# Optimization experiments

Hardware: AMD Instinct MI355X
Metric: run time of the kernel (lower is better)

The kernel has to match this reference:

```python
import jax, jax.numpy as jnp
import numpy as np
import math

D_MODEL = 1024
H = 16
D_K = D_MODEL // H
D_FF = 4096
EPS = 1e-6


def layer_norm(x, gamma, beta):
    # torch LayerNorm-variant: unbiased std, eps added to std (not var)
    mean = jnp.mean(x, axis=-1, keepdims=True)
    std = jnp.std(x, axis=-1, keepdims=True, ddof=1)
    return gamma * (x - mean) / (std + EPS) + beta


def mha(x, mask, w_q, w_k, w_v, w_o):
    B, S, _ = x.shape
    # torch Linear (no bias): y = x @ W.T
    q = (x @ w_q.T).reshape(B, S, H, D_K).transpose(0, 2, 1, 3)
    k = (x @ w_k.T).reshape(B, S, H, D_K).transpose(0, 2, 1, 3)
    v = (x @ w_v.T).reshape(B, S, H, D_K).transpose(0, 2, 1, 3)
    scores = jnp.einsum('bhqd,bhkd->bhqk', q, k) / math.sqrt(D_K)
    scores = jnp.where(mask == 0, jnp.float32(-1e9), scores)
    attn = jax.nn.softmax(scores, axis=-1)
    out = jnp.einsum('bhqk,bhkd->bhqd', attn, v)
    out = out.transpose(0, 2, 1, 3).reshape(B, S, D_MODEL)
    return out @ w_o.T


def setup_inputs() -> dict:
    key = jax.random.key(0)
    ks = jax.random.split(key, 12)
    B, S = 4, 2048
    s = 0.02
    return {
        'x': jax.random.normal(ks[0], (B, S, D_MODEL), jnp.float32),
        'src_mask': jnp.ones((B, 1, 1, S), jnp.int32),
        'w_q': jax.random.normal(ks[1], (D_MODEL, D_MODEL), jnp.float32) * s,
        'w_k': jax.random.normal(ks[2], (D_MODEL, D_MODEL), jnp.float32) * s,
        'w_v': jax.random.normal(ks[3], (D_MODEL, D_MODEL), jnp.float32) * s,
        'w_o': jax.random.normal(ks[4], (D_MODEL, D_MODEL), jnp.float32) * s,
        'w1': jax.random.normal(ks[5], (D_FF, D_MODEL), jnp.float32) * s,
        'b1': jnp.zeros((D_FF,), jnp.float32),
        'w2': jax.random.normal(ks[6], (D_MODEL, D_FF), jnp.float32) * s,
        'b2': jnp.zeros((D_MODEL,), jnp.float32),
        'gamma1': jnp.ones((D_MODEL,), jnp.float32),
        'beta1': jnp.zeros((D_MODEL,), jnp.float32),
        'gamma2': jnp.ones((D_MODEL,), jnp.float32),
        'beta2': jnp.zeros((D_MODEL,), jnp.float32),
    }


def reference(x, src_mask, w_q, w_k, w_v, w_o, w1, b1, w2, b2,
              gamma1, beta1, gamma2, beta2):
    # AddNorm1: x + MHA(LN(x))  (pre-norm, dropout=0)
    x = x + mha(layer_norm(x, gamma1, beta1), src_mask, w_q, w_k, w_v, w_o)
    # AddNorm2: x + FFN(LN(x))
    h = layer_norm(x, gamma2, beta2)
    ffn = jax.nn.relu(h @ w1.T + b1) @ w2.T + b2
    return x + ffn
```

## Files before the change

kernel.cpp:

```cpp
#include <hip/hip_runtime.h>

#define D_MODEL 1024
#define NH 16
#define DK 64
#define DFF 4096
#define SEQ 2048
#define BATCH 4
#define NROWS (BATCH*SEQ)
#define CHUNK 2048
#define NCHUNK (NROWS/CHUNK)

typedef short bf16x8 __attribute__((ext_vector_type(8)));
typedef float f32x4 __attribute__((ext_vector_type(4)));

__device__ __forceinline__ float bf2f(unsigned short u){
  union { float f; unsigned int i; } x; x.i = ((unsigned int)u) << 16; return x.f;
}
__device__ __forceinline__ unsigned short f2bf(float f){
  union { float f; unsigned int i; } x; x.f = f;
  unsigned int r = x.i + 0x7fffu + ((x.i >> 16) & 1u);
  return (unsigned short)(r >> 16);
}
__device__ __forceinline__ float fexp2(float x){
#if __has_builtin(__builtin_amdgcn_exp2f)
  return __builtin_amdgcn_exp2f(x);
#else
  return __exp2f(x);
#endif
}

__device__ __forceinline__ void gl_lds16(const void* g, void* l) {
  __builtin_amdgcn_global_load_lds((const __attribute__((address_space(1))) void*)g,
                                   (__attribute__((address_space(3))) void*)l, 16, 0, 0);
}

__global__ __launch_bounds__(256) void cvt_f2b(const float* __restrict__ in,
                                               unsigned short* __restrict__ out, int n)
{
  int i = (blockIdx.x * 256 + threadIdx.x) * 4;
  if (i < n) {
    float4 f = *(const float4*)(in + i);
    union { int2 v; unsigned short u[4]; } o;
    o.u[0] = f2bf(f.x); o.u[1] = f2bf(f.y); o.u[2] = f2bf(f.z); o.u[3] = f2bf(f.w);
    *(int2*)(out + i) = o.v;
  }
}

__global__ __launch_bounds__(256) void ln_kernel(const float* __restrict__ in,
    const float* __restrict__ gam, const float* __restrict__ bet,
    unsigned short* __restrict__ out)
{
  const int row = blockIdx.x, t = threadIdx.x;
  const int base = t * 4;
  float4 raw = *(const float4*)(in + (size_t)row * D_MODEL + base);
  float v[4] = { raw.x, raw.y, raw.z, raw.w };
  float s  = v[0] + v[1] + v[2] + v[3];
  float s2 = v[0]*v[0] + v[1]*v[1] + v[2]*v[2] + v[3]*v[3];
  #pragma unroll
  for (int off = 32; off > 0; off >>= 1) {
    s  += __shfl_down(s,  off);
    s2 += __shfl_down(s2, off);
  }
  __shared__ float red[10];
  const int wid = t >> 6, lane = t & 63;
  if (lane == 0) { red[wid] = s; red[4 + wid] = s2; }
  __syncthreads();
  if (t == 0) {
    float ts  = red[0] + red[1] + red[2] + red[3];
    float ts2 = red[4] + red[5] + red[6] + red[7];
    float mean = ts * (1.0f / D_MODEL);
    float var  = (ts2 - (float)D_MODEL * mean * mean) * (1.0f / (D_MODEL - 1));
    var = fmaxf(var, 0.0f);
    red[8] = mean;
    red[9] = 1.0f / (sqrtf(var) + 1e-6f);
  }
  __syncthreads();
  const float mean = red[8], inv = red[9];
  float4 g4 = *(const float4*)(gam + base);
  float4 b4 = *(const float4*)(bet + base);
  union { int2 v; unsigned short u[4]; } o;
  o.u[0] = f2bf(g4.x * (v[0] - mean) * inv + b4.x);
  o.u[1] = f2bf(g4.y * (v[1] - mean) * inv + b4.y);
  o.u[2] = f2bf(g4.z * (v[2] - mean) * inv + b4.z);
  o.u[3] = f2bf(g4.w * (v[3] - mean) * inv + b4.w);
  *(int2*)(out + (size_t)row * D_MODEL + base) = o.v;
}

__global__ __launch_bounds__(256) void gemm_bt(
    const unsigned short* __restrict__ A,
    const unsigned short* __restrict__ Bw,
    int K, int N, int sA, int sB,
    const float* __restrict__ bias,
    int relu,
    const float* __restrict__ residf,
    unsigned short* __restrict__ outb,
    float* __restrict__ outf,
    float* __restrict__ atomf,
    unsigned short* __restrict__ outq,
    unsigned short* __restrict__ outk,
    unsigned short* __restrict__ outvt)
{
  __shared__ __attribute__((aligned(16))) short sAm[128 * 32];
  __shared__ __attribute__((aligned(16))) short sBm[128 * 32];
  const int t = threadIdx.x;
  const int tileN = blockIdx.x * 128;
  const int tileM = blockIdx.y * 128;
  const int kz = blockIdx.z;
  const size_t koff = (size_t)kz * K;
  const int wid = t >> 6, lane = t & 63;
  const int wM = (wid >> 1) * 64, wN = (wid & 1) * 64;
  const int quad = lane >> 4, lrow = lane & 15;

  f32x4 acc[4][4] = {};

  for (int k0 = 0; k0 < K; k0 += 32) {
    #pragma unroll
    for (int it = 0; it < 2; it++) {
      int seg = it * 256 + t;
      int row = seg >> 2, c8 = (seg & 3) * 8;
      gl_lds16(A  + (size_t)(tileM + row) * sA + koff + k0 + c8, &sAm[seg * 8]);
      gl_lds16(Bw + (size_t)(tileN + row) * sB + koff + k0 + c8, &sBm[seg * 8]);
    }
    __syncthreads();
    bf16x8 af[4], bfr[4];
    #pragma unroll
    for (int i = 0; i < 4; i++) {
      af[i]  = *(const bf16x8*)&sAm[(wM + i * 16 + lrow) * 32 + quad * 8];
      bfr[i] = *(const bf16x8*)&sBm[(wN + i * 16 + lrow) * 32 + quad * 8];
    }
    #pragma unroll
    for (int i = 0; i < 4; i++)
      #pragma unroll
      for (int j = 0; j < 4; j++)
        acc[i][j] = __builtin_amdgcn_mfma_f32_16x16x32_bf16(af[i], bfr[j], acc[i][j], 0, 0, 0);
    __syncthreads();
  }

  unsigned short* qk_out = nullptr;
  int qkv_cat = 0;
  if (outq) {
    qkv_cat = tileN >> 10;
    qk_out = (qkv_cat == 0) ? outq : outk;
  }

  #pragma unroll
  for (int i = 0; i < 4; i++) {
    #pragma unroll
    for (int j = 0; j < 4; j++) {
      const int col  = tileN + wN + j * 16 + lrow;
      const int row0 = tileM + wM + i * 16 + quad * 4;
      const float bv = (bias && kz == 0) ? bias[col] : 0.0f;
      float vals[4];
      #pragma unroll
      for (int r = 0; r < 4; r++) {
        float val = acc[i][j][r] + bv;
        if (relu) val = fmaxf(val, 0.0f);
        if (residf) val += residf[(size_t)(row0 + r) * N + col];
        vals[r] = val;
      }
      if (outq) {
        const int lcol = col & 1023;
        if (qkv_cat < 2) {
          #pragma unroll
          for (int r = 0; r < 4; r++)
            qk_out[(size_t)(row0 + r) * D_MODEL + lcol] = f2bf(vals[r]);
        } else {
          union { int2 v; unsigned short u[4]; } pk;
          #pragma unroll
          for (int r = 0; r < 4; r++) pk.u[r] = f2bf(vals[r]);
          size_t tidx = (((size_t)(row0 >> 11) * NH + (lcol >> 6)) * DK + (lcol & 63)) * SEQ + (row0 & 2047);
          *(int2*)(outvt + tidx) = pk.v;
        }
      } else if (atomf) {
        #pragma unroll
        for (int r = 0; r < 4; r++)
          atomicAdd(&atomf[(size_t)(row0 + r) * N + col], vals[r]);
      } else {
        #pragma unroll
        for (int r = 0; r < 4; r++) {
          const size_t idx = (size_t)(row0 + r) * N + col;
          if (outf) outf[idx] = vals[r];
          if (outb) outb[idx] = f2bf(vals[r]);
        }
      }
    }
  }
}

#define AQT 64
#define AKT 64
__global__ __launch_bounds__(256) void attn_mfma(
    const unsigned short* __restrict__ Qg,
    const unsigned short* __restrict__ Kg,
    const unsigned short* __restrict__ Vt,
    const int* __restrict__ mask,
    unsigned short* __restrict__ Og)
{
  __shared__ __attribute__((aligned(16))) short Ks[AKT * 64];
  __shared__ __attribute__((aligned(16))) short Vs[DK * 64];
  __shared__ __attribute__((aligned(16))) short Ps[AQT * 64];
  __shared__ __attribute__((aligned(16))) float maddf[AKT];

  const int bid = blockIdx.x;
  const int nqt = SEQ / AQT;
  const int b  = bid / (NH * nqt);
  const int h  = (bid / nqt) % NH;
  const int q0 = (bid % nqt) * AQT;
  const int t  = threadIdx.x;
  const int wv = t >> 6, lane = t & 63;
  const int quad = lane >> 4, l15 = lane & 15;
  const int sw = (l15 & 7) << 3;
  const float SCL = 0.125f * 1.44269504f;

  bf16x8 qf0, qf1;
  {
    const unsigned short* qrow = Qg + (size_t)(b * SEQ + q0 + wv * 16 + l15) * D_MODEL + h * DK;
    qf0 = *(const bf16x8*)(qrow + quad * 8);
    qf1 = *(const bf16x8*)(qrow + 32 + quad * 8);
  }
  f32x4 oacc[4] = {};
  float m_run = -1e30f, l_run = 0.0f;

  const unsigned short* Kbase = Kg + (size_t)(b * SEQ) * D_MODEL + h * DK;
  const unsigned short* Vbase = Vt + ((size_t)(b * NH + h) * DK) * SEQ;

  for (int kt = 0; kt < SEQ; kt += AKT) {
    #pragma unroll
    for (int it = 0; it < 2; it++) {
      int s = it * 256 + t;
      int row = s >> 3;
      int scol = ((s & 7) * 8) ^ ((row & 7) << 3);
      gl_lds16(Kbase + (size_t)(kt + row) * D_MODEL + scol, &Ks[s * 8]);
      gl_lds16(Vbase + (size_t)row * SEQ + kt + scol, &Vs[s * 8]);
    }
    if (t < AKT) maddf[t] = mask[b * SEQ + kt + t] ? 0.0f : -1.0e9f;
    __syncthreads();

    f32x4 sc[4];
    #pragma unroll
    for (int ct = 0; ct < 4; ct++) {
      const int krow = ct * 16 + l15;
      bf16x8 kb0 = *(const bf16x8*)&Ks[krow * 64 + ((quad * 8) ^ sw)];
      bf16x8 kb1 = *(const bf16x8*)&Ks[krow * 64 + ((32 + quad * 8) ^ sw)];
      f32x4 a = {};
      a = __builtin_amdgcn_mfma_f32_16x16x32_bf16(kb0, qf0, a, 0, 0, 0);
      a = __builtin_amdgcn_mfma_f32_16x16x32_bf16(kb1, qf1, a, 0, 0, 0);
      f32x4 md = *(const f32x4*)&maddf[ct * 16 + quad * 4];
      #pragma unroll
      for (int r = 0; r < 4; r++) a[r] = a[r] * SCL + md[r];
      sc[ct] = a;
    }

    float tmax = sc[0][0];
    #pragma unroll
    for (int ct = 0; ct < 4; ct++)
      #pragma unroll
      for (int r = 0; r < 4; r++) tmax = fmaxf(tmax, sc[ct][r]);
    tmax = fmaxf(tmax, __shfl_xor(tmax, 16));
    tmax = fmaxf(tmax, __shfl_xor(tmax, 32));

    if (!__all(tmax - m_run <= 11.5415603f)) {
      float mn = fmaxf(m_run, tmax);
      float alpha = fexp2(m_run - mn);
      m_run = mn;
      l_run *= alpha;
      float a4[4];
      #pragma unroll
      for (int r = 0; r < 4; r++) a4[r] = __shfl(alpha, quad * 4 + r);
      #pragma unroll
      for (int dt = 0; dt < 4; dt++)
        #pragma unroll
        for (int r = 0; r < 4; r++) oacc[dt][r] *= a4[r];
    }

    const int prow = wv * 16 + l15;
    float rs = 0.0f;
    #pragma unroll
    for (int ct = 0; ct < 4; ct++) {
      float p0 = fexp2(sc[ct][0] - m_run);
      float p1 = fexp2(sc[ct][1] - m_run);
      float p2 = fexp2(sc[ct][2] - m_run);
      float p3 = fexp2(sc[ct][3] - m_run);
      rs += (p0 + p1) + (p2 + p3);
      unsigned int lo, hi;
      asm("v_cvt_pk_bf16_f32 %0, %1, %2" : "=v"(lo) : "v"(p0), "v"(p1));
      asm("v_cvt_pk_bf16_f32 %0, %1, %2" : "=v"(hi) : "v"(p2), "v"(p3));
      int2 pv; pv.x = (int)lo; pv.y = (int)hi;
      *(int2*)&Ps[prow * 64 + ((ct * 16 + quad * 4) ^ sw)] = pv;
    }
    rs += __shfl_xor(rs, 16);
    rs += __shfl_xor(rs, 32);
    l_run += rs;

    bf16x8 pf0 = *(const bf16x8*)&Ps[prow * 64 + ((quad * 8) ^ sw)];
    bf16x8 pf1 = *(const bf16x8*)&Ps[prow * 64 + ((32 + quad * 8) ^ sw)];
    #pragma unroll
    for (int dt = 0; dt < 4; dt++) {
      const int vrow = dt * 16 + l15;
      bf16x8 vb0 = *(const bf16x8*)&Vs[vrow * 64 + ((quad * 8) ^ sw)];
      bf16x8 vb1 = *(const bf16x8*)&Vs[vrow * 64 + ((32 + quad * 8) ^ sw)];
      oacc[dt] = __builtin_amdgcn_mfma_f32_16x16x32_bf16(pf0, vb0, oacc[dt], 0, 0, 0);
      oacc[dt] = __builtin_amdgcn_mfma_f32_16x16x32_bf16(pf1, vb1, oacc[dt], 0, 0, 0);
    }
    __syncthreads();
  }

  float li = 1.0f / l_run;
  float linv4[4];
  #pragma unroll
  for (int r = 0; r < 4; r++) linv4[r] = __shfl(li, quad * 4 + r);
  #pragma unroll
  for (int dt = 0; dt < 4; dt++)
    #pragma unroll
    for (int r = 0; r < 4; r++)
      Og[(size_t)(b * SEQ + q0 + wv * 16 + quad * 4 + r) * D_MODEL + h * DK + dt * 16 + l15] =
        f2bf(oacc[dt][r] * linv4[r]);
}

extern "C" void kernel_launch(void* const* d_in, const int* in_sizes, int n_in,
                              void* d_out, int out_size, void* d_ws, size_t ws_size,
                              hipStream_t stream)
{
  (void)in_sizes; (void)n_in; (void)out_size; (void)ws_size;
  const float* x   = (const float*)d_in[0];
  const int*   msk = (const int*)d_in[1];
  const float* w_q = (const float*)d_in[2];
  const float* w_k = (const float*)d_in[3];
  const float* w_v = (const float*)d_in[4];
  const float* w_o = (const float*)d_in[5];
  const float* w1  = (const float*)d_in[6];
  const float* b1  = (const float*)d_in[7];
  const float* w2  = (const float*)d_in[8];
  const float* b2  = (const float*)d_in[9];
  const float* g1  = (const float*)d_in[10];
  const float* be1 = (const float*)d_in[11];
  const float* g2  = (const float*)d_in[12];
  const float* be2 = (const float*)d_in[13];
  float* outf = (float*)d_out;

  char* ws = (char*)d_ws;
  const size_t MB = 1024 * 1024;
  unsigned short* q_b  = (unsigned short*)(ws + 0);
  unsigned short* k_b  = (unsigned short*)(ws + 16 * MB);
  unsigned short* vt_b = (unsigned short*)(ws + 32 * MB);
  unsigned short* wo16 = (unsigned short*)(ws + 16 * MB);
  unsigned short* w116 = (unsigned short*)(ws + 0);
  unsigned short* w216 = (unsigned short*)(ws + 8 * MB);
  unsigned short* ln2b = vt_b;
  unsigned short* hffc = k_b;

  unsigned short* ln1b   = (unsigned short*)d_out;
  unsigned short* wqkv16 = (unsigned short*)d_out + 8 * 1024 * 1024;

  dim3 blk(256);
  const int nw = D_MODEL * D_MODEL;
  const int nf = DFF * D_MODEL;

  cvt_f2b<<<nw / 1024, blk, 0, stream>>>(w_q, wqkv16, nw);
  cvt_f2b<<<nw / 1024, blk, 0, stream>>>(w_k, wqkv16 + nw, nw);
  cvt_f2b<<<nw / 1024, blk, 0, stream>>>(w_v, wqkv16 + 2 * nw, nw);
  ln_kernel<<<NROWS, blk, 0, stream>>>(x, g1, be1, ln1b);

  dim3 gqkv(3 * D_MODEL / 128, NROWS / 128);
  gemm_bt<<<gqkv, blk, 0, stream>>>(ln1b, wqkv16, D_MODEL, 3 * D_MODEL, D_MODEL, D_MODEL,
                                    nullptr, 0, nullptr, nullptr, nullptr, nullptr,
                                    q_b, k_b, vt_b);

  attn_mfma<<<BATCH * NH * (SEQ / AQT), blk, 0, stream>>>(q_b, k_b, vt_b, msk, q_b);

  cvt_f2b<<<nw / 1024, blk, 0, stream>>>(w_o, wo16, nw);
  dim3 gN1024(D_MODEL / 128, NROWS / 128);
  gemm_bt<<<gN1024, blk, 0, stream>>>(q_b, wo16, D_MODEL, D_MODEL, D_MODEL, D_MODEL,
                                      nullptr, 0, x, nullptr, outf, nullptr,
                                      nullptr, nullptr, nullptr);

  cvt_f2b<<<nf / 1024, blk, 0, stream>>>(w1, w116, nf);
  cvt_f2b<<<nf / 1024, blk, 0, stream>>>(w2, w216, nf);
  ln_kernel<<<NROWS, blk, 0, stream>>>(outf, g2, be2, ln2b);
  for (int c = 0; c < NCHUNK; c++) {
    const size_t ro = (size_t)c * CHUNK;
    dim3 g1c(DFF / 128,     CHUNK / 128);
    dim3 g2c(D_MODEL / 128, CHUNK / 128, 4);
    gemm_bt<<<g1c, blk, 0, stream>>>(ln2b + ro * D_MODEL, w116, D_MODEL, DFF,
                                     D_MODEL, D_MODEL, b1, 1,
                                     nullptr, hffc, nullptr, nullptr,
                                     nullptr, nullptr, nullptr);
    gemm_bt<<<g2c, blk, 0, stream>>>(hffc, w216, DFF / 4, D_MODEL, DFF, DFF, b2, 0,
                                     nullptr, nullptr, nullptr, outf + ro * D_MODEL,
                                     nullptr, nullptr, nullptr);
  }
}
```

Baseline: 774.3 us.

## Double-buffer GEMM LDS, swizzle blocks across XCDs, read attention K/V directly

After: 1.044 ms. 1.35x slower.

```diff
diff --git a/kernel.cpp b/kernel.cpp
--- a/kernel.cpp
+++ b/kernel.cpp
@@ -34,6 +34,10 @@
                                    (__attribute__((address_space(3))) void*)l, 16, 0, 0);
 }
 
+__device__ __forceinline__ int xcd_swz(int hid, int total) {
+  return (hid & 7) * (total >> 3) + (hid >> 3);
+}
+
 __global__ __launch_bounds__(256) void cvt_f2b(const float* __restrict__ in,
                                                unsigned short* __restrict__ out, int n)
 {
@@ -44,6 +48,13 @@
     o.u[0] = f2bf(f.x); o.u[1] = f2bf(f.y); o.u[2] = f2bf(f.z); o.u[3] = f2bf(f.w);
     *(int2*)(out + i) = o.v;
   }
+}
+
+__global__ __launch_bounds__(256) void mask2f(const int* __restrict__ m,
+                                              float* __restrict__ o, int n)
+{
+  int i = blockIdx.x * 256 + threadIdx.x;
+  if (i < n) o[i] = m[i] ? 0.0f : -1.0e9f;
 }
 
 __global__ __launch_bounds__(256) void ln_kernel(const float* __restrict__ in,
@@ -86,7 +97,7 @@
   *(int2*)(out + (size_t)row * D_MODEL + base) = o.v;
 }
 
-__global__ __launch_bounds__(256) void gemm_bt(
+__global__ __launch_bounds__(256, 4) void gemm_bt(
     const unsigned short* __restrict__ A,
     const unsigned short* __restrict__ Bw,
     int K, int N, int sA, int sB,
@@ -100,11 +111,15 @@
     unsigned short* __restrict__ outk,
     unsigned short* __restrict__ outvt)
 {
-  __shared__ __attribute__((aligned(16))) short sAm[128 * 32];
-  __shared__ __attribute__((aligned(16))) short sBm[128 * 32];
+  __shared__ __attribute__((aligned(16))) short sA0[128 * 32];
+  __shared__ __attribute__((aligned(16))) short sA1[128 * 32];
+  __shared__ __attribute__((aligned(16))) short sB0[128 * 32];
+  __shared__ __attribute__((aligned(16))) short sB1[128 * 32];
   const int t = threadIdx.x;
-  const int tileN = blockIdx.x * 128;
-  const int tileM = blockIdx.y * 128;
+  const int lid  = xcd_swz(blockIdx.y * gridDim.x + blockIdx.x,
+                           gridDim.x * gridDim.y);
+  const int tileN = (lid % gridDim.x) * 128;
+  const int tileM = (lid / gridDim.x) * 128;
   const int kz = blockIdx.z;
   const size_t koff = (size_t)kz * K;
   const int wid = t >> 6, lane = t & 63;
@@ -113,26 +128,40 @@
 
   f32x4 acc[4][4] = {};
 
-  for (int k0 = 0; k0 < K; k0 += 32) {
-    #pragma unroll
-    for (int it = 0; it < 2; it++) {
-      int seg = it * 256 + t;
-      int row = seg >> 2, c8 = (seg & 3) * 8;
-      gl_lds16(A  + (size_t)(tileM + row) * sA + koff + k0 + c8, &sAm[seg * 8]);
-      gl_lds16(Bw + (size_t)(tileN + row) * sB + koff + k0 + c8, &sBm[seg * 8]);
-    }
-    __syncthreads();
+  const unsigned short* pa = A  + (size_t)(tileM + (t >> 2)) * sA + koff + (t & 3) * 8;
+  const unsigned short* pb = Bw + (size_t)(tileN + (t >> 2)) * sB + koff + (t & 3) * 8;
+  const size_t a64 = (size_t)64 * sA, b64 = (size_t)64 * sB;
+
+  auto stageTo = [&](short* dA, short* dB) {
+    gl_lds16(pa,       dA + t * 8);
+    gl_lds16(pa + a64, dA + (256 + t) * 8);
+    gl_lds16(pb,       dB + t * 8);
+    gl_lds16(pb + b64, dB + (256 + t) * 8);
+    pa += 32; pb += 32;
+  };
+  auto compute = [&](const short* cA, const short* cB) {
     bf16x8 af[4], bfr[4];
     #pragma unroll
     for (int i = 0; i < 4; i++) {
-      af[i]  = *(const bf16x8*)&sAm[(wM + i * 16 + lrow) * 32 + quad * 8];
-      bfr[i] = *(const bf16x8*)&sBm[(wN + i * 16 + lrow) * 32 + quad * 8];
+      af[i]  = *(const bf16x8*)&cA[(wM + i * 16 + lrow) * 32 + quad * 8];
+      bfr[i] = *(const bf16x8*)&cB[(wN + i * 16 + lrow) * 32 + quad * 8];
     }
     #pragma unroll
     for (int i = 0; i < 4; i++)
       #pragma unroll
       for (int j = 0; j < 4; j++)
         acc[i][j] = __builtin_amdgcn_mfma_f32_16x16x32_bf16(af[i], bfr[j], acc[i][j], 0, 0, 0);
+  };
+
+  const int nk = K >> 5;
+  stageTo(sA0, sB0);
+  __syncthreads();
+  for (int ik = 0; ik < nk; ik += 2) {
+    if (ik + 1 < nk) stageTo(sA1, sB1);
+    compute(sA0, sB0);
+    __syncthreads();
+    if (ik + 2 < nk) stageTo(sA0, sB0);
+    compute(sA1, sB1);
     __syncthreads();
   }
 
@@ -193,15 +222,12 @@
     const unsigned short* __restrict__ Qg,
     const unsigned short* __restrict__ Kg,
     const unsigned short* __restrict__ Vt,
-    const int* __restrict__ mask,
+    const float* __restrict__ maddg,
     unsigned short* __restrict__ Og)
 {
-  __shared__ __attribute__((aligned(16))) short Ks[AKT * 64];
-  __shared__ __attribute__((aligned(16))) short Vs[DK * 64];
-  __shared__ __attribute__((aligned(16))) short Ps[AQT * 64];
-  __shared__ __attribute__((aligned(16))) float maddf[AKT];
-
-  const int bid = blockIdx.x;
+  __shared__ __attribute__((aligned(16))) short Ps[64 * 64];
+
+  const int bid = xcd_swz(blockIdx.x, gridDim.x);
   const int nqt = SEQ / AQT;
   const int b  = bid / (NH * nqt);
   const int h  = (bid / nqt) % NH;
@@ -214,48 +240,42 @@
 
   bf16x8 qf0, qf1;
   {
-    const unsigned short* qrow = Qg + (size_t)(b * SEQ + q0 + wv * 16 + l15) * D_MODEL + h * DK;
+    const unsigned short* qrow =
+        Qg + (size_t)(b * SEQ + q0 + wv * 16 + l15) * D_MODEL + h * DK;
     qf0 = *(const bf16x8*)(qrow + quad * 8);
     qf1 = *(const bf16x8*)(qrow + 32 + quad * 8);
   }
   f32x4 oacc[4] = {};
   float m_run = -1e30f, l_run = 0.0f;
 
-  const unsigned short* Kbase = Kg + (size_t)(b * SEQ) * D_MODEL + h * DK;
-  const unsigned short* Vbase = Vt + ((size_t)(b * NH + h) * DK) * SEQ;
+  const unsigned short* kfrag =
+      Kg + (size_t)(b * SEQ + l15) * D_MODEL + h * DK + quad * 8;
+  const unsigned short* vfrag =
+      Vt + ((size_t)(b * NH + h) * DK + l15) * SEQ + quad * 8;
+  const float* mg = maddg + b * SEQ + quad * 4;
+  const int prow = wv * 16 + l15;
 
   for (int kt = 0; kt < SEQ; kt += AKT) {
-    #pragma unroll
-    for (int it = 0; it < 2; it++) {
-      int s = it * 256 + t;
-      int row = s >> 3;
-      int scol = ((s & 7) * 8) ^ ((row & 7) << 3);
-      gl_lds16(Kbase + (size_t)(kt + row) * D_MODEL + scol, &Ks[s * 8]);
-      gl_lds16(Vbase + (size_t)row * SEQ + kt + scol, &Vs[s * 8]);
-    }
-    if (t < AKT) maddf[t] = mask[b * SEQ + kt + t] ? 0.0f : -1.0e9f;
-    __syncthreads();
-
     f32x4 sc[4];
     #pragma unroll
     for (int ct = 0; ct < 4; ct++) {
-      const int krow = ct * 16 + l15;
-      bf16x8 kb0 = *(const bf16x8*)&Ks[krow * 64 + ((quad * 8) ^ sw)];
-      bf16x8 kb1 = *(const bf16x8*)&Ks[krow * 64 + ((32 + quad * 8) ^ sw)];
+      const unsigned short* kr = kfrag + (size_t)(kt + ct * 16) * D_MODEL;
+      bf16x8 kb0 = *(const bf16x8*)(kr);
+      bf16x8 kb1 = *(const bf16x8*)(kr + 32);
       f32x4 a = {};
       a = __builtin_amdgcn_mfma_f32_16x16x32_bf16(kb0, qf0, a, 0, 0, 0);
       a = __builtin_amdgcn_mfma_f32_16x16x32_bf16(kb1, qf1, a, 0, 0, 0);
-      f32x4 md = *(const f32x4*)&maddf[ct * 16 + quad * 4];
+      f32x4 md = *(const f32x4*)(mg + kt + ct * 16);
       #pragma unroll
       for (int r = 0; r < 4; r++) a[r] = a[r] * SCL + md[r];
       sc[ct] = a;
     }
 
-    float tmax = sc[0][0];
-    #pragma unroll
-    for (int ct = 0; ct < 4; ct++)
-      #pragma unroll
-      for (int r = 0; r < 4; r++) tmax = fmaxf(tmax, sc[ct][r]);
+    float tmax = fmaxf(fmaxf(sc[0][0], sc[0][1]), fmaxf(sc[0][2], sc[0][3]));
+    #pragma unroll
+    for (int ct = 1; ct < 4; ct++)
+      tmax = fmaxf(tmax, fmaxf(fmaxf(sc[ct][0], sc[ct][1]),
+                               fmaxf(sc[ct][2], sc[ct][3])));
     tmax = fmaxf(tmax, __shfl_xor(tmax, 16));
     tmax = fmaxf(tmax, __shfl_xor(tmax, 32));
 
@@ -273,7 +293,6 @@
         for (int r = 0; r < 4; r++) oacc[dt][r] *= a4[r];
     }
 
-    const int prow = wv * 16 + l15;
     float rs = 0.0f;
     #pragma unroll
     for (int ct = 0; ct < 4; ct++) {
@@ -296,13 +315,12 @@
     bf16x8 pf1 = *(const bf16x8*)&Ps[prow * 64 + ((32 + quad * 8) ^ sw)];
     #pragma unroll
     for (int dt = 0; dt < 4; dt++) {
-      const int vrow = dt * 16 + l15;
-      bf16x8 vb0 = *(const bf16x8*)&Vs[vrow * 64 + ((quad * 8) ^ sw)];
-      bf16x8 vb1 = *(const bf16x8*)&Vs[vrow * 64 + ((32 + quad * 8) ^ sw)];
+      const unsigned short* vr = vfrag + (size_t)(dt * 16) * SEQ + kt;
+      bf16x8 vb0 = *(const bf16x8*)(vr);
+      bf16x8 vb1 = *(const bf16x8*)(vr + 32);
       oacc[dt] = __builtin_amdgcn_mfma_f32_16x16x32_bf16(pf0, vb0, oacc[dt], 0, 0, 0);
       oacc[dt] = __builtin_amdgcn_mfma_f32_16x16x32_bf16(pf1, vb1, oacc[dt], 0, 0, 0);
     }
-    __syncthreads();
   }
 
   float li = 1.0f / l_run;
@@ -348,6 +366,7 @@
   unsigned short* w216 = (unsigned short*)(ws + 8 * MB);
   unsigned short* ln2b = vt_b;
   unsigned short* hffc = k_b;
+  float* maddg = (float*)(ws + 48 * MB);
 
   unsigned short* ln1b   = (unsigned short*)d_out;
   unsigned short* wqkv16 = (unsigned short*)d_out + 8 * 1024 * 1024;
@@ -359,6 +378,7 @@
   cvt_f2b<<<nw / 1024, blk, 0, stream>>>(w_q, wqkv16, nw);
   cvt_f2b<<<nw / 1024, blk, 0, stream>>>(w_k, wqkv16 + nw, nw);
   cvt_f2b<<<nw / 1024, blk, 0, stream>>>(w_v, wqkv16 + 2 * nw, nw);
+  mask2f<<<NROWS / 256, blk, 0, stream>>>(msk, maddg, NROWS);
   ln_kernel<<<NROWS, blk, 0, stream>>>(x, g1, be1, ln1b);
 
   dim3 gqkv(3 * D_MODEL / 128, NROWS / 128);
@@ -366,7 +386,7 @@
                                     nullptr, 0, nullptr, nullptr, nullptr, nullptr,
                                     q_b, k_b, vt_b);
 
-  attn_mfma<<<BATCH * NH * (SEQ / AQT), blk, 0, stream>>>(q_b, k_b, vt_b, msk, q_b);
+  attn_mfma<<<BATCH * NH * (SEQ / AQT), blk, 0, stream>>>(q_b, k_b, vt_b, maddg, q_b);
 
   cvt_f2b<<<nw / 1024, blk, 0, stream>>>(w_o, wo16, nw);
   dim3 gN1024(D_MODEL / 128, NROWS / 128);
```
